# Kernel tuning notes

Hardware: AMD Instinct MI355X
Metric: run time of the kernel (lower is better)

Reference implementation:

```python
import jax, jax.numpy as jnp
import numpy as np

H, F = 128, 16  # hidden_dim, input_dim per init_kwargs
B, S = 1024, 64


def setup_inputs() -> dict:
    key = jax.random.key(0)
    ks = jax.random.split(key, 7)
    def lin(k, shape, fan_in):
        return jax.random.uniform(k, shape, jnp.float32, -1.0, 1.0) / np.sqrt(fan_in).astype(np.float32)
    return {
        "x": jax.random.normal(ks[0], (B, S, F), jnp.float32),
        # CDEFunc net: Linear(H,H) -> Tanh -> Linear(H, H*F)
        "W1": lin(ks[1], (H, H), H), "b1": lin(ks[2], (H,), H),
        "W2": lin(ks[3], (H * F, H), H), "b2": lin(ks[4], (H * F,), H),
        # init_linear: Linear(F, H)
        "Wi": lin(ks[5], (H, F), F), "bi": lin(ks[6], (H,), F),
    }


def _hermite_coeffs(x, times):
    """Hermite cubic with backward differences (torchcde). Returns per-interval
    derivative-polynomial coeffs: dX(f) = b + 2c f + 3d f^2, f in [0, dt]."""
    dt = times[1:] - times[:-1]                      # [S-1]
    dtv = dt[None, :, None]
    p0, p1 = x[:, :-1], x[:, 1:]
    seg = (p1 - p0) / dtv                            # chord slopes [B,S-1,F]
    # knot derivative i = backward difference (slope of segment i-1); knot 0 uses segment 0
    m0 = jnp.concatenate([seg[:, :1], seg[:, :-1]], axis=1)
    m1 = seg
    c = (3.0 * seg - (2.0 * m0 + m1)) / dtv
    d = (-2.0 * seg + (m0 + m1)) / (dtv * dtv)
    return m0, c, d, dt


def reference(x, W1, b1, W2, b2, Wi, bi):
    Bb, Ss, Ff = x.shape
    times = jnp.linspace(0.0, 1.0, Ss, dtype=x.dtype)
    bcoef, ccoef, dcoef, dt = _hermite_coeffs(x, times)

    def fnet(h):  # [B,H] -> [B,H,F]
        z = jnp.tanh(h @ W1.T + b1)
        return (z @ W2.T + b2).reshape(Bb, H, Ff)

    def g(dX, h):  # dh/dt = f(h) @ dX/dt : [B,H,F] . [B,F] -> [B,H]
        return jnp.einsum('bhf,bf->bh', fnet(h), dX)

    h0 = x[:, 0] @ Wi.T + bi  # [B,H]

    def step(h, per_interval):
        bi_, ci_, di_, dti = per_interval
        def dX(f):
            return bi_ + (2.0 * ci_ + 3.0 * di_ * f) * f
        # torchdiffeq 'rk4' = RK4 3/8 rule, one step per grid interval
        k1 = g(dX(0.0), h)
        k2 = g(dX(dti / 3.0), h + dti * k1 / 3.0)
        k3 = g(dX(2.0 * dti / 3.0), h + dti * (k2 - k1 / 3.0))
        k4 = g(dX(dti), h + dti * (k1 - k2 + k3))
        return h + dti * (k1 + 3.0 * (k2 + k3) + k4) * 0.125, None

    xs = (jnp.moveaxis(bcoef, 1, 0), jnp.moveaxis(ccoef, 1, 0), jnp.moveaxis(dcoef, 1, 0), dt)
    hT, _ = jax.lax.scan(step, h0, xs)
    return hT  # [B,H]
```

## Files before the change

### kernel.cpp

```cpp
#include <hip/hip_runtime.h>


#define NT 1024

__global__ void pack_w2_kernel(const float* __restrict__ W2, float4* __restrict__ PW2) {
    const int q = blockIdx.x * blockDim.x + threadIdx.x;
    const int t = q & 1023, j = (q >> 10) & 1, kc = q >> 11;
    PW2[q] = *(const float4*)&W2[((t * 2 + j) << 7) + (kc << 2)];
}

template<bool PACKED>
__global__ __launch_bounds__(NT) void cde_kernel(
    const float* __restrict__ x,  const float* __restrict__ W1,
    const float* __restrict__ b1, const float* __restrict__ W2,
    const float* __restrict__ b2, const float* __restrict__ Wi,
    const float* __restrict__ bi, const float4* __restrict__ PW2,
    float* __restrict__ out)
{
    __shared__ float pW1[32 * 128 * 4];
    __shared__ float sx[4 * 64 * 16];
    __shared__ float zB[4 * 128];
    __shared__ float hB[4 * 128];
    __shared__ float hsB[4 * 128];
    __shared__ float skS[4 * 4 * 128];
    __shared__ float sdX[4 * 4 * 16];

    const int t = threadIdx.x;
    const int b_base = blockIdx.x * 4;
    const float dt = 1.0f / 63.0f, rdt = 63.0f;

    for (int idx = t; idx < 4096; idx += NT) sx[idx] = x[(size_t)b_base * 1024 + idx];
    for (int idx = t; idx < 16384; idx += NT) {
        const int j4 = idx >> 9, k = (idx >> 2) & 127, jj = idx & 3;
        pW1[idx] = W1[k * 128 + j4 * 4 + jj];
    }
    __syncthreads();

    if (t < 512) {
        const int j = t & 127, b = t >> 7;
        float acc = bi[j];
#pragma unroll
        for (int f = 0; f < 16; ++f) acc = fmaf(Wi[j * 16 + f], sx[b * 1024 + f], acc);
        hB[b * 128 + j] = acc;
        hsB[b * 128 + j] = acc;
    }
    const float kb1 = (t < 512) ? b1[t & 127] : 0.0f;
    const float2 bb = *(const float2*)&b2[t * 2];
    const float4* pw  = PW2 + t;
    const float4* r0p = (const float4*)W2 + t * 64;
    const float4* r1p = r0p + 32;
    __syncthreads();

    for (int i = 0; i < 63; ++i) {
        if (t < 256) {
            const int f = t & 15, b = (t >> 4) & 3, s = t >> 6;
            const float* xb = &sx[b * 1024];
            const float x0  = xb[i * 16 + f];
            const float x1  = xb[(i + 1) * 16 + f];
            const float seg = (x1 - x0) * rdt;
            const float m0  = (i == 0) ? seg : (x0 - xb[(i - 1) * 16 + f]) * rdt;
            const float c   = (2.0f * seg - 2.0f * m0) * rdt;
            const float d   = (m0 - seg) * rdt * rdt;
            const float ft  = (float)s * (dt * (1.0f / 3.0f));
            sdX[(s * 4 + b) * 16 + f] = fmaf(fmaf(3.0f * d, ft, 2.0f * c), ft, m0);
        }

        for (int s = 0; s < 4; ++s) {
            if (t < 512) {
                const int k = t & 127, b = t >> 7;
                float acc = kb1;
#pragma unroll 8
                for (int j4 = 0; j4 < 32; ++j4) {
                    const float4 w = *(const float4*)&pW1[(j4 * 128 + k) * 4];
                    const float4 h = *(const float4*)&hsB[b * 128 + j4 * 4];
                    acc = fmaf(w.x, h.x, acc); acc = fmaf(w.y, h.y, acc);
                    acc = fmaf(w.z, h.z, acc); acc = fmaf(w.w, h.w, acc);
                }
                zB[b * 128 + k] = tanhf(acc);
            }
            __syncthreads();

            {
                float a[2][4];
#pragma unroll
                for (int j = 0; j < 2; ++j)
#pragma unroll
                    for (int b = 0; b < 4; ++b) a[j][b] = 0.0f;

                float4 w0 = PACKED ? pw[0]    : r0p[0];
                float4 w1 = PACKED ? pw[1024] : r1p[0];
#pragma unroll 2
                for (int kc = 0; kc < 32; ++kc) {
                    const float4 cw0 = w0, cw1 = w1;
                    if (kc < 31) {
                        if (PACKED) { w0 = pw[(kc + 1) * 2048]; w1 = pw[(kc + 1) * 2048 + 1024]; }
                        else        { w0 = r0p[kc + 1];          w1 = r1p[kc + 1]; }
                    }
#pragma unroll
                    for (int b = 0; b < 4; ++b) {
                        const float4 z = *(const float4*)&zB[b * 128 + kc * 4];
                        a[0][b] = fmaf(cw0.x, z.x, a[0][b]);
                        a[0][b] = fmaf(cw0.y, z.y, a[0][b]);
                        a[0][b] = fmaf(cw0.z, z.z, a[0][b]);
                        a[0][b] = fmaf(cw0.w, z.w, a[0][b]);
                        a[1][b] = fmaf(cw1.x, z.x, a[1][b]);
                        a[1][b] = fmaf(cw1.y, z.y, a[1][b]);
                        a[1][b] = fmaf(cw1.z, z.z, a[1][b]);
                        a[1][b] = fmaf(cw1.w, z.w, a[1][b]);
                    }
                }
                const int fp = t & 7, hh = t >> 3;
                float kv[4];
#pragma unroll
                for (int b = 0; b < 4; ++b) {
                    const float2 dx2 = *(const float2*)&sdX[(s * 4 + b) * 16 + fp * 2];
                    kv[b] = (a[0][b] + bb.x) * dx2.x + (a[1][b] + bb.y) * dx2.y;
                }
#pragma unroll
                for (int b = 0; b < 4; ++b) {
                    kv[b] += __shfl_xor(kv[b], 1);
                    kv[b] += __shfl_xor(kv[b], 2);
                    kv[b] += __shfl_xor(kv[b], 4);
                }
                if (fp == 0) {
#pragma unroll
                    for (int b = 0; b < 4; ++b) skS[(s * 4 + b) * 128 + hh] = kv[b];
                }
            }
            __syncthreads();

            if (t < 512) {
                const int j = t & 127, b = t >> 7;
                const float k1 = skS[(0 * 4 + b) * 128 + j];
                if (s == 3) {
                    const float k2 = skS[(1 * 4 + b) * 128 + j];
                    const float k3 = skS[(2 * 4 + b) * 128 + j];
                    const float k4 = skS[(3 * 4 + b) * 128 + j];
                    const float nh = hB[b * 128 + j]
                                   + dt * 0.125f * (k1 + 3.0f * (k2 + k3) + k4);
                    hB[b * 128 + j]  = nh;
                    hsB[b * 128 + j] = nh;
                } else {
                    const float hv = hB[b * 128 + j];
                    float nh;
                    if (s == 0) {
                        nh = fmaf(dt * (1.0f / 3.0f), k1, hv);
                    } else if (s == 1) {
                        const float k2 = skS[(1 * 4 + b) * 128 + j];
                        nh = hv + dt * k2 - (dt * (1.0f / 3.0f)) * k1;
                    } else {
                        const float k2 = skS[(1 * 4 + b) * 128 + j];
                        const float k3 = skS[(2 * 4 + b) * 128 + j];
                        nh = fmaf(dt, (k1 - k2 + k3), hv);
                    }
                    hsB[b * 128 + j] = nh;
                }
            }
            __syncthreads();
        }
    }

    if (t < 512) {
        const int j = t & 127, b = t >> 7;
        out[(size_t)(b_base + b) * 128 + j] = hB[b * 128 + j];
    }
}

extern "C" void kernel_launch(void* const* d_in, const int* in_sizes, int n_in,
                              void* d_out, int out_size, void* d_ws, size_t ws_size,
                              hipStream_t stream)
{
    (void)in_sizes; (void)n_in; (void)out_size;
    const float* x  = (const float*)d_in[0];
    const float* W1 = (const float*)d_in[1];
    const float* b1 = (const float*)d_in[2];
    const float* W2 = (const float*)d_in[3];
    const float* b2 = (const float*)d_in[4];
    const float* Wi = (const float*)d_in[5];
    const float* bi = (const float*)d_in[6];
    float* o = (float*)d_out;
    float4* PW2 = (float4*)d_ws;
    const bool packed = (ws_size >= (size_t)(2048 * 128 * 4));

    if (packed) {
        hipLaunchKernelGGL(pack_w2_kernel, dim3(256), dim3(256), 0, stream, W2, PW2);
        hipLaunchKernelGGL(HIP_KERNEL_NAME(cde_kernel<true>), dim3(256), dim3(NT), 0, stream,
                           x, W1, b1, W2, b2, Wi, bi, PW2, o);
    } else {
        hipLaunchKernelGGL(HIP_KERNEL_NAME(cde_kernel<false>), dim3(256), dim3(NT), 0, stream,
                           x, W1, b1, W2, b2, Wi, bi, PW2, o);
    }
}
```

Before: 3.276 ms.

## Fuse RK stage-state update into W1 matvec, keep W2 slices in registers, cut barriers

Removes the separate per-stage hidden-state update pass by recomputing the stage input (h plus k combinations) inside the W1 matvec. All 1024 threads now share the W1 matvec, split across two half-waves and combined with a shuffle, instead of only 512. The number of barriers per RK stage drops from three to two, and they use a custom LDS-only waitcnt+s_barrier. Six W2 float4 chunks per thread stay resident in registers across iterations, and the prefetch wraps around, which reduces global/L2 traffic. The cost is higher register pressure under launch_bounds(1024,4) and redundant recomputation of stage inputs.

```diff
diff --git a/kernel.cpp b/kernel.cpp
--- a/kernel.cpp
+++ b/kernel.cpp
@@ -2,6 +2,7 @@
 
 
 #define NT 1024
+#define PERSIST 6
 
 __global__ void pack_w2_kernel(const float* __restrict__ W2, float4* __restrict__ PW2) {
     const int q = blockIdx.x * blockDim.x + threadIdx.x;
@@ -9,25 +10,29 @@
     PW2[q] = *(const float4*)&W2[((t * 2 + j) << 7) + (kc << 2)];
 }
 
+__device__ __forceinline__ void lgkm_barrier() {
+    asm volatile("s_waitcnt lgkmcnt(0)\n\ts_barrier" ::: "memory");
+}
+
 template<bool PACKED>
-__global__ __launch_bounds__(NT) void cde_kernel(
+__global__ __launch_bounds__(NT, 4) void cde_kernel(
     const float* __restrict__ x,  const float* __restrict__ W1,
     const float* __restrict__ b1, const float* __restrict__ W2,
     const float* __restrict__ b2, const float* __restrict__ Wi,
     const float* __restrict__ bi, const float4* __restrict__ PW2,
     float* __restrict__ out)
 {
-    __shared__ float pW1[32 * 128 * 4];
-    __shared__ float sx[4 * 64 * 16];
-    __shared__ float zB[4 * 128];
-    __shared__ float hB[4 * 128];
-    __shared__ float hsB[4 * 128];
-    __shared__ float skS[4 * 4 * 128];
-    __shared__ float sdX[4 * 4 * 16];
+    __shared__ float pW1[16384];
+    __shared__ float sx[4096];
+    __shared__ float zB[512];
+    __shared__ float hB[512];
+    __shared__ float skS[2048];
+    __shared__ float sdX[256];
 
     const int t = threadIdx.x;
     const int b_base = blockIdx.x * 4;
     const float dt = 1.0f / 63.0f, rdt = 63.0f;
+    const float c13 = dt * (1.0f / 3.0f);
 
     for (int idx = t; idx < 4096; idx += NT) sx[idx] = x[(size_t)b_base * 1024 + idx];
     for (int idx = t; idx < 16384; idx += NT) {
@@ -42,71 +47,111 @@
 #pragma unroll
         for (int f = 0; f < 16; ++f) acc = fmaf(Wi[j * 16 + f], sx[b * 1024 + f], acc);
         hB[b * 128 + j] = acc;
-        hsB[b * 128 + j] = acc;
-    }
-    const float kb1 = (t < 512) ? b1[t & 127] : 0.0f;
+    }
+
+    const int w = t >> 6, l = t & 63;
+    const int gb   = w >> 2;
+    const int gk   = ((w & 3) << 5) | (l & 31);
+    const int jh16 = (l >> 5) << 4;
+    const float b1v = b1[gk];
     const float2 bb = *(const float2*)&b2[t * 2];
+
     const float4* pw  = PW2 + t;
     const float4* r0p = (const float4*)W2 + t * 64;
     const float4* r1p = r0p + 32;
+
+    float4 wra[PERSIST], wrb[PERSIST];
+#pragma unroll
+    for (int kc = 0; kc < PERSIST; ++kc) {
+        if (PACKED) { wra[kc] = pw[kc * 2048]; wrb[kc] = pw[kc * 2048 + 1024]; }
+        else        { wra[kc] = r0p[kc];       wrb[kc] = r1p[kc]; }
+    }
+    float4 na = PACKED ? pw[PERSIST * 2048]        : r0p[PERSIST];
+    float4 nb = PACKED ? pw[PERSIST * 2048 + 1024] : r1p[PERSIST];
     __syncthreads();
 
     for (int i = 0; i < 63; ++i) {
-        if (t < 256) {
-            const int f = t & 15, b = (t >> 4) & 3, s = t >> 6;
-            const float* xb = &sx[b * 1024];
-            const float x0  = xb[i * 16 + f];
-            const float x1  = xb[(i + 1) * 16 + f];
-            const float seg = (x1 - x0) * rdt;
-            const float m0  = (i == 0) ? seg : (x0 - xb[(i - 1) * 16 + f]) * rdt;
-            const float c   = (2.0f * seg - 2.0f * m0) * rdt;
-            const float d   = (m0 - seg) * rdt * rdt;
-            const float ft  = (float)s * (dt * (1.0f / 3.0f));
-            sdX[(s * 4 + b) * 16 + f] = fmaf(fmaf(3.0f * d, ft, 2.0f * c), ft, m0);
-        }
-
+#pragma unroll
         for (int s = 0; s < 4; ++s) {
-            if (t < 512) {
-                const int k = t & 127, b = t >> 7;
-                float acc = kb1;
-#pragma unroll 8
-                for (int j4 = 0; j4 < 32; ++j4) {
-                    const float4 w = *(const float4*)&pW1[(j4 * 128 + k) * 4];
-                    const float4 h = *(const float4*)&hsB[b * 128 + j4 * 4];
-                    acc = fmaf(w.x, h.x, acc); acc = fmaf(w.y, h.y, acc);
-                    acc = fmaf(w.z, h.z, acc); acc = fmaf(w.w, h.w, acc);
-                }
-                zB[b * 128 + k] = tanhf(acc);
+            if (s == 0 && t < 256) {
+                const int f = t & 15, b = (t >> 4) & 3, sn = t >> 6;
+                const float* xb = &sx[b * 1024];
+                const float x0  = xb[i * 16 + f];
+                const float x1  = xb[(i + 1) * 16 + f];
+                const float seg = (x1 - x0) * rdt;
+                const float m0  = (i == 0) ? seg : (x0 - xb[(i - 1) * 16 + f]) * rdt;
+                const float c   = (2.0f * seg - 2.0f * m0) * rdt;
+                const float d   = (m0 - seg) * rdt * rdt;
+                const float ft  = (float)sn * c13;
+                sdX[(sn * 4 + b) * 16 + f] = fmaf(fmaf(3.0f * d, ft, 2.0f * c), ft, m0);
             }
-            __syncthreads();
-
             {
-                float a[2][4];
-#pragma unroll
-                for (int j = 0; j < 2; ++j)
-#pragma unroll
-                    for (int b = 0; b < 4; ++b) a[j][b] = 0.0f;
-
-                float4 w0 = PACKED ? pw[0]    : r0p[0];
-                float4 w1 = PACKED ? pw[1024] : r1p[0];
-#pragma unroll 2
-                for (int kc = 0; kc < 32; ++kc) {
-                    const float4 cw0 = w0, cw1 = w1;
-                    if (kc < 31) {
-                        if (PACKED) { w0 = pw[(kc + 1) * 2048]; w1 = pw[(kc + 1) * 2048 + 1024]; }
-                        else        { w0 = r0p[kc + 1];          w1 = r1p[kc + 1]; }
+                float acc = 0.0f;
+                const float* wp  = &pW1[(jh16 * 128 + gk) * 4];
+                const float* hp  = &hB[gb * 128 + jh16 * 4];
+                const float* k1p = &skS[(0 * 4 + gb) * 128 + jh16 * 4];
+                const float* k2p = &skS[(1 * 4 + gb) * 128 + jh16 * 4];
+                const float* k3p = &skS[(2 * 4 + gb) * 128 + jh16 * 4];
+#pragma unroll
+                for (int u = 0; u < 16; ++u) {
+                    const float4 wv = *(const float4*)&wp[u * 512];
+                    const float4 hv = *(const float4*)&hp[u * 4];
+                    float hx = hv.x, hy = hv.y, hz = hv.z, hw = hv.w;
+                    if (s == 1) {
+                        const float4 k1 = *(const float4*)&k1p[u * 4];
+                        hx = fmaf(c13, k1.x, hx); hy = fmaf(c13, k1.y, hy);
+                        hz = fmaf(c13, k1.z, hz); hw = fmaf(c13, k1.w, hw);
+                    } else if (s == 2) {
+                        const float4 k1 = *(const float4*)&k1p[u * 4];
+                        const float4 k2 = *(const float4*)&k2p[u * 4];
+                        hx = fmaf(dt, k2.x, fmaf(-c13, k1.x, hx));
+                        hy = fmaf(dt, k2.y, fmaf(-c13, k1.y, hy));
+                        hz = fmaf(dt, k2.z, fmaf(-c13, k1.z, hz));
+                        hw = fmaf(dt, k2.w, fmaf(-c13, k1.w, hw));
+                    } else if (s == 3) {
+                        const float4 k1 = *(const float4*)&k1p[u * 4];
+                        const float4 k2 = *(const float4*)&k2p[u * 4];
+                        const float4 k3 = *(const float4*)&k3p[u * 4];
+                        hx = fmaf(dt, k1.x - k2.x + k3.x, hx);
+                        hy = fmaf(dt, k1.y - k2.y + k3.y, hy);
+                        hz = fmaf(dt, k1.z - k2.z + k3.z, hz);
+                        hw = fmaf(dt, k1.w - k2.w + k3.w, hw);
                     }
+                    acc = fmaf(wv.x, hx, acc); acc = fmaf(wv.y, hy, acc);
+                    acc = fmaf(wv.z, hz, acc); acc = fmaf(wv.w, hw, acc);
+                }
+                acc += __shfl_xor(acc, 32);
+                const float zv = tanhf(acc + b1v);
+                if (l < 32) zB[gb * 128 + gk] = zv;
+            }
+            lgkm_barrier();
+
+            {
+                float a0[4] = {0.f, 0.f, 0.f, 0.f}, a1[4] = {0.f, 0.f, 0.f, 0.f};
+#pragma unroll
+                for (int kc = 0; kc < PERSIST; ++kc) {
 #pragma unroll
                     for (int b = 0; b < 4; ++b) {
                         const float4 z = *(const float4*)&zB[b * 128 + kc * 4];
-                        a[0][b] = fmaf(cw0.x, z.x, a[0][b]);
-                        a[0][b] = fmaf(cw0.y, z.y, a[0][b]);
-                        a[0][b] = fmaf(cw0.z, z.z, a[0][b]);
-                        a[0][b] = fmaf(cw0.w, z.w, a[0][b]);
-                        a[1][b] = fmaf(cw1.x, z.x, a[1][b]);
-                        a[1][b] = fmaf(cw1.y, z.y, a[1][b]);
-                        a[1][b] = fmaf(cw1.z, z.z, a[1][b]);
-                        a[1][b] = fmaf(cw1.w, z.w, a[1][b]);
+                        a0[b] = fmaf(wra[kc].x, z.x, a0[b]); a0[b] = fmaf(wra[kc].y, z.y, a0[b]);
+                        a0[b] = fmaf(wra[kc].z, z.z, a0[b]); a0[b] = fmaf(wra[kc].w, z.w, a0[b]);
+                        a1[b] = fmaf(wrb[kc].x, z.x, a1[b]); a1[b] = fmaf(wrb[kc].y, z.y, a1[b]);
+                        a1[b] = fmaf(wrb[kc].z, z.z, a1[b]); a1[b] = fmaf(wrb[kc].w, z.w, a1[b]);
+                    }
+                }
+#pragma unroll
+                for (int kc = PERSIST; kc < 32; ++kc) {
+                    const float4 ca = na, cb = nb;
+                    const int nk = (kc == 31) ? PERSIST : kc + 1;
+                    if (PACKED) { na = pw[nk * 2048]; nb = pw[nk * 2048 + 1024]; }
+                    else        { na = r0p[nk];       nb = r1p[nk]; }
+#pragma unroll
+                    for (int b = 0; b < 4; ++b) {
+                        const float4 z = *(const float4*)&zB[b * 128 + kc * 4];
+                        a0[b] = fmaf(ca.x, z.x, a0[b]); a0[b] = fmaf(ca.y, z.y, a0[b]);
+                        a0[b] = fmaf(ca.z, z.z, a0[b]); a0[b] = fmaf(ca.w, z.w, a0[b]);
+                        a1[b] = fmaf(cb.x, z.x, a1[b]); a1[b] = fmaf(cb.y, z.y, a1[b]);
+                        a1[b] = fmaf(cb.z, z.z, a1[b]); a1[b] = fmaf(cb.w, z.w, a1[b]);
                     }
                 }
                 const int fp = t & 7, hh = t >> 3;
@@ -114,10 +159,7 @@
 #pragma unroll
                 for (int b = 0; b < 4; ++b) {
                     const float2 dx2 = *(const float2*)&sdX[(s * 4 + b) * 16 + fp * 2];
-                    kv[b] = (a[0][b] + bb.x) * dx2.x + (a[1][b] + bb.y) * dx2.y;
-                }
-#pragma unroll
-                for (int b = 0; b < 4; ++b) {
+                    kv[b] = (a0[b] + bb.x) * dx2.x + (a1[b] + bb.y) * dx2.y;
                     kv[b] += __shfl_xor(kv[b], 1);
                     kv[b] += __shfl_xor(kv[b], 2);
                     kv[b] += __shfl_xor(kv[b], 4);
@@ -127,37 +169,17 @@
                     for (int b = 0; b < 4; ++b) skS[(s * 4 + b) * 128 + hh] = kv[b];
                 }
             }
-            __syncthreads();
-
-            if (t < 512) {
-                const int j = t & 127, b = t >> 7;
-                const float k1 = skS[(0 * 4 + b) * 128 + j];
-                if (s == 3) {
-                    const float k2 = skS[(1 * 4 + b) * 128 + j];
-                    const float k3 = skS[(2 * 4 + b) * 128 + j];
-                    const float k4 = skS[(3 * 4 + b) * 128 + j];
-                    const float nh = hB[b * 128 + j]
-                                   + dt * 0.125f * (k1 + 3.0f * (k2 + k3) + k4);
-                    hB[b * 128 + j]  = nh;
-                    hsB[b * 128 + j] = nh;
-                } else {
-                    const float hv = hB[b * 128 + j];
-                    float nh;
-                    if (s == 0) {
-                        nh = fmaf(dt * (1.0f / 3.0f), k1, hv);
-                    } else if (s == 1) {
-                        const float k2 = skS[(1 * 4 + b) * 128 + j];
-                        nh = hv + dt * k2 - (dt * (1.0f / 3.0f)) * k1;
-                    } else {
-                        const float k2 = skS[(1 * 4 + b) * 128 + j];
-                        const float k3 = skS[(2 * 4 + b) * 128 + j];
-                        nh = fmaf(dt, (k1 - k2 + k3), hv);
-                    }
-                    hsB[b * 128 + j] = nh;
-                }
-            }
-            __syncthreads();
+            lgkm_barrier();
         }
+        if (t < 512) {
+            const int j = t & 127, b = t >> 7;
+            const float k1 = skS[(0 * 4 + b) * 128 + j];
+            const float k2 = skS[(1 * 4 + b) * 128 + j];
+            const float k3 = skS[(2 * 4 + b) * 128 + j];
+            const float k4 = skS[(3 * 4 + b) * 128 + j];
+            hB[b * 128 + j] = fmaf(dt * 0.125f, k1 + 3.0f * (k2 + k3) + k4, hB[b * 128 + j]);
+        }
+        lgkm_barrier();
     }
 
     if (t < 512) {
```

Measured after the change: 7.289 ms. 122% more time.

## Split W1 GEMV across all threads, fast tanh, and reorder packed W2 layout

Applied to the files above, without the earlier changes.

The first-layer matvec now uses all 1024 threads instead of 512: each output is split over two half-waves that each handle 16 float4 chunks, then combined with a cross-lane shuffle. tanhf is replaced by an exp2/rcp approximation with clamping. The packed W2 layout is reorganised per wavefront, so each wave reads a contiguous region, and the first W2 loads are issued before the barrier. The stage loop is fully unrolled and the dX computation moves inside it. The fast tanh gives slightly different rounding from tanhf.

```diff
diff --git a/kernel.cpp b/kernel.cpp
--- a/kernel.cpp
+++ b/kernel.cpp
@@ -5,8 +5,16 @@
 
 __global__ void pack_w2_kernel(const float* __restrict__ W2, float4* __restrict__ PW2) {
     const int q = blockIdx.x * blockDim.x + threadIdx.x;
-    const int t = q & 1023, j = (q >> 10) & 1, kc = q >> 11;
-    PW2[q] = *(const float4*)&W2[((t * 2 + j) << 7) + (kc << 2)];
+    const int lane = q & 63, c = (q >> 6) & 63, w = q >> 12;
+    const int kc = c >> 1, j = c & 1;
+    const int t = (w << 6) | lane;
+    PW2[q] = *(const float4*)&W2[((2 * t + j) << 7) + (kc << 2)];
+}
+
+__device__ __forceinline__ float fast_tanh(float x) {
+    const float xc = fminf(fmaxf(x, -9.0f), 9.0f);
+    const float e  = __builtin_amdgcn_exp2f(xc * 2.88539008177792681472f);
+    return 1.0f - 2.0f * __builtin_amdgcn_rcpf(e + 1.0f);
 }
 
 template<bool PACKED>
@@ -17,17 +25,18 @@
     const float* __restrict__ bi, const float4* __restrict__ PW2,
     float* __restrict__ out)
 {
-    __shared__ float pW1[32 * 128 * 4];
-    __shared__ float sx[4 * 64 * 16];
-    __shared__ float zB[4 * 128];
-    __shared__ float hB[4 * 128];
-    __shared__ float hsB[4 * 128];
-    __shared__ float skS[4 * 4 * 128];
-    __shared__ float sdX[4 * 4 * 16];
+    __shared__ float pW1[16384];
+    __shared__ float sx[4096];
+    __shared__ float zB[512];
+    __shared__ float hB[512];
+    __shared__ float hsB[512];
+    __shared__ float skS[2048];
+    __shared__ float sdX[256];
 
     const int t = threadIdx.x;
     const int b_base = blockIdx.x * 4;
     const float dt = 1.0f / 63.0f, rdt = 63.0f;
+    const float c13 = dt * (1.0f / 3.0f);
 
     for (int idx = t; idx < 4096; idx += NT) sx[idx] = x[(size_t)b_base * 1024 + idx];
     for (int idx = t; idx < 16384; idx += NT) {
@@ -41,72 +50,73 @@
         float acc = bi[j];
 #pragma unroll
         for (int f = 0; f < 16; ++f) acc = fmaf(Wi[j * 16 + f], sx[b * 1024 + f], acc);
-        hB[b * 128 + j] = acc;
+        hB[b * 128 + j]  = acc;
         hsB[b * 128 + j] = acc;
     }
-    const float kb1 = (t < 512) ? b1[t & 127] : 0.0f;
+
+    const int w = t >> 6, l = t & 63;
+    const int g1b  = w >> 2;
+    const int g1k  = ((w & 3) << 5) | (l & 31);
+    const int jh16 = (l >> 5) << 4;
+    const float b1v = b1[g1k];
     const float2 bb = *(const float2*)&b2[t * 2];
-    const float4* pw  = PW2 + t;
+
+    const float4* pb  = PW2 + (w << 12) + l;
     const float4* r0p = (const float4*)W2 + t * 64;
     const float4* r1p = r0p + 32;
     __syncthreads();
 
     for (int i = 0; i < 63; ++i) {
-        if (t < 256) {
-            const int f = t & 15, b = (t >> 4) & 3, s = t >> 6;
-            const float* xb = &sx[b * 1024];
-            const float x0  = xb[i * 16 + f];
-            const float x1  = xb[(i + 1) * 16 + f];
-            const float seg = (x1 - x0) * rdt;
-            const float m0  = (i == 0) ? seg : (x0 - xb[(i - 1) * 16 + f]) * rdt;
-            const float c   = (2.0f * seg - 2.0f * m0) * rdt;
-            const float d   = (m0 - seg) * rdt * rdt;
-            const float ft  = (float)s * (dt * (1.0f / 3.0f));
-            sdX[(s * 4 + b) * 16 + f] = fmaf(fmaf(3.0f * d, ft, 2.0f * c), ft, m0);
-        }
-
+#pragma unroll
         for (int s = 0; s < 4; ++s) {
-            if (t < 512) {
-                const int k = t & 127, b = t >> 7;
-                float acc = kb1;
-#pragma unroll 8
-                for (int j4 = 0; j4 < 32; ++j4) {
-                    const float4 w = *(const float4*)&pW1[(j4 * 128 + k) * 4];
-                    const float4 h = *(const float4*)&hsB[b * 128 + j4 * 4];
-                    acc = fmaf(w.x, h.x, acc); acc = fmaf(w.y, h.y, acc);
-                    acc = fmaf(w.z, h.z, acc); acc = fmaf(w.w, h.w, acc);
-                }
-                zB[b * 128 + k] = tanhf(acc);
-            }
+            if (s == 0 && t < 256) {
+                const int f = t & 15, b = (t >> 4) & 3, sn = t >> 6;
+                const float* xb = &sx[b * 1024];
+                const float x0  = xb[i * 16 + f];
+                const float x1  = xb[(i + 1) * 16 + f];
+                const float seg = (x1 - x0) * rdt;
+                const float m0  = (i == 0) ? seg : (x0 - xb[(i - 1) * 16 + f]) * rdt;
+                const float c   = (2.0f * seg - 2.0f * m0) * rdt;
+                const float d   = (m0 - seg) * rdt * rdt;
+                const float ft  = (float)sn * c13;
+                sdX[(sn * 4 + b) * 16 + f] = fmaf(fmaf(3.0f * d, ft, 2.0f * c), ft, m0);
+            }
+            {
+                float acc = 0.0f;
+                const float* wp = &pW1[(jh16 * 128 + g1k) * 4];
+                const float* hp = &hsB[g1b * 128 + jh16 * 4];
+#pragma unroll
+                for (int u = 0; u < 16; ++u) {
+                    const float4 wv = *(const float4*)&wp[u * 512];
+                    const float4 hv = *(const float4*)&hp[u * 4];
+                    acc = fmaf(wv.x, hv.x, acc); acc = fmaf(wv.y, hv.y, acc);
+                    acc = fmaf(wv.z, hv.z, acc); acc = fmaf(wv.w, hv.w, acc);
+                }
+                acc += __shfl_xor(acc, 32);
+                const float zv = fast_tanh(acc + b1v);
+                if (l < 32) zB[g1b * 128 + g1k] = zv;
+            }
+            float4 w0, w1;
+            if (PACKED) { w0 = pb[0];  w1 = pb[64]; }
+            else        { w0 = r0p[0]; w1 = r1p[0]; }
             __syncthreads();
 
             {
-                float a[2][4];
-#pragma unroll
-                for (int j = 0; j < 2; ++j)
-#pragma unroll
-                    for (int b = 0; b < 4; ++b) a[j][b] = 0.0f;
-
-                float4 w0 = PACKED ? pw[0]    : r0p[0];
-                float4 w1 = PACKED ? pw[1024] : r1p[0];
-#pragma unroll 2
+                float a0[4] = {0.f,0.f,0.f,0.f}, a1[4] = {0.f,0.f,0.f,0.f};
+#pragma unroll
                 for (int kc = 0; kc < 32; ++kc) {
-                    const float4 cw0 = w0, cw1 = w1;
+                    const float4 ca = w0, cb = w1;
                     if (kc < 31) {
-                        if (PACKED) { w0 = pw[(kc + 1) * 2048]; w1 = pw[(kc + 1) * 2048 + 1024]; }
-                        else        { w0 = r0p[kc + 1];          w1 = r1p[kc + 1]; }
+                        if (PACKED) { w0 = pb[(kc + 1) * 128]; w1 = pb[(kc + 1) * 128 + 64]; }
+                        else        { w0 = r0p[kc + 1];        w1 = r1p[kc + 1]; }
                     }
 #pragma unroll
                     for (int b = 0; b < 4; ++b) {
                         const float4 z = *(const float4*)&zB[b * 128 + kc * 4];
-                        a[0][b] = fmaf(cw0.x, z.x, a[0][b]);
-                        a[0][b] = fmaf(cw0.y, z.y, a[0][b]);
-                        a[0][b] = fmaf(cw0.z, z.z, a[0][b]);
-                        a[0][b] = fmaf(cw0.w, z.w, a[0][b]);
-                        a[1][b] = fmaf(cw1.x, z.x, a[1][b]);
-                        a[1][b] = fmaf(cw1.y, z.y, a[1][b]);
-                        a[1][b] = fmaf(cw1.z, z.z, a[1][b]);
-                        a[1][b] = fmaf(cw1.w, z.w, a[1][b]);
+                        a0[b] = fmaf(ca.x, z.x, a0[b]); a0[b] = fmaf(ca.y, z.y, a0[b]);
+                        a0[b] = fmaf(ca.z, z.z, a0[b]); a0[b] = fmaf(ca.w, z.w, a0[b]);
+                        a1[b] = fmaf(cb.x, z.x, a1[b]); a1[b] = fmaf(cb.y, z.y, a1[b]);
+                        a1[b] = fmaf(cb.z, z.z, a1[b]); a1[b] = fmaf(cb.w, z.w, a1[b]);
                     }
                 }
                 const int fp = t & 7, hh = t >> 3;
@@ -114,10 +124,7 @@
 #pragma unroll
                 for (int b = 0; b < 4; ++b) {
                     const float2 dx2 = *(const float2*)&sdX[(s * 4 + b) * 16 + fp * 2];
-                    kv[b] = (a[0][b] + bb.x) * dx2.x + (a[1][b] + bb.y) * dx2.y;
-                }
-#pragma unroll
-                for (int b = 0; b < 4; ++b) {
+                    kv[b] = (a0[b] + bb.x) * dx2.x + (a1[b] + bb.y) * dx2.y;
                     kv[b] += __shfl_xor(kv[b], 1);
                     kv[b] += __shfl_xor(kv[b], 2);
                     kv[b] += __shfl_xor(kv[b], 4);
@@ -144,10 +151,10 @@
                     const float hv = hB[b * 128 + j];
                     float nh;
                     if (s == 0) {
-                        nh = fmaf(dt * (1.0f / 3.0f), k1, hv);
+                        nh = fmaf(c13, k1, hv);
                     } else if (s == 1) {
                         const float k2 = skS[(1 * 4 + b) * 128 + j];
-                        nh = hv + dt * k2 - (dt * (1.0f / 3.0f)) * k1;
+                        nh = hv + dt * k2 - c13 * k1;
                     } else {
                         const float k2 = skS[(1 * 4 + b) * 128 + j];
                         const float k3 = skS[(2 * 4 + b) * 128 + j];
```

Measured after the change: 6.194 ms. 1.89x slower.
